# Kernel tuning notes

Hardware: AMD Instinct MI355X
Metric: run time of the kernel (lower is better)

## Reference

```python
import jax, jax.numpy as jnp
import numpy as np

B, N, K, C = 4, 8192, 16, 128
T = 3  # num_iterations


def _gather(x, idx):
    # x: (B, N, C), idx: (B, N, K) -> (B, N, K, C)
    return jax.vmap(lambda a, i: a[i])(x, idx)


def _linear(x, W, b):
    # torch nn.Linear convention: W is (out, in)
    return x @ W.T + b


def setup_inputs() -> dict:
    key = jax.random.key(0)
    ks = jax.random.split(key, 20)
    s = 0.05
    inp = {
        'xyz': jax.random.normal(ks[0], (B, N, 3), jnp.float32),
        'features': jax.random.normal(ks[1], (B, N, C), jnp.float32),
        'knn_idx': jax.random.randint(ks[2], (B, N, K), 0, N),
        # offset_pred: Linear(C,C) -> ReLU -> Linear(C,3)
        'off_W1': jax.random.normal(ks[3], (C, C), jnp.float32) * s,
        'off_b1': jnp.zeros((C,), jnp.float32),
        'off_W2': jax.random.normal(ks[4], (3, C), jnp.float32) * s,
        'off_b2': jnp.zeros((3,), jnp.float32),
        # per-iteration edge MLP: Linear(3+C, C) -> ReLU -> Linear(C, C)
        'edge_W1': jax.random.normal(ks[5], (T, C, 3 + C), jnp.float32) * s,
        'edge_b1': jnp.zeros((T, C), jnp.float32),
        'edge_W2': jax.random.normal(ks[6], (T, C, C), jnp.float32) * s,
        'edge_b2': jnp.zeros((T, C), jnp.float32),
        # per-iteration update MLP: Linear(2C, C) -> ReLU -> Linear(C, C)
        'upd_W1': jax.random.normal(ks[7], (T, C, 2 * C), jnp.float32) * s,
        'upd_b1': jnp.zeros((T, C), jnp.float32),
        'upd_W2': jax.random.normal(ks[8], (T, C, C), jnp.float32) * s,
        'upd_b2': jnp.zeros((T, C), jnp.float32),
    }
    return inp


def reference(xyz, features, knn_idx, off_W1, off_b1, off_W2, off_b2,
              edge_W1, edge_b1, edge_W2, edge_b2,
              upd_W1, upd_b1, upd_W2, upd_b2):
    n_iter = edge_W1.shape[0]
    for t in range(n_iter):
        delta_xyz = _linear(jax.nn.relu(_linear(features, off_W1, off_b1)), off_W2, off_b2)
        neighbor_xyz = _gather(xyz, knn_idx)          # (B,N,K,3)
        neighbor_feat = _gather(features, knn_idx)    # (B,N,K,C)
        center_xyz = xyz + delta_xyz                  # (B,N,3)
        rel_pos = neighbor_xyz - center_xyz[:, :, None, :]
        edge_input = jnp.concatenate([rel_pos, neighbor_feat], axis=-1)  # (B,N,K,3+C)
        edge_feat = _linear(jax.nn.relu(_linear(edge_input, edge_W1[t], edge_b1[t])), edge_W2[t], edge_b2[t])
        agg_feat = jnp.max(edge_feat, axis=2)         # (B,N,C)
        upd_in = jnp.concatenate([agg_feat, features], axis=-1)
        features = features + _linear(jax.nn.relu(_linear(upd_in, upd_W1[t], upd_b1[t])), upd_W2[t], upd_b2[t])
    return features
```

## Files before the change

### kernel.cpp

```cpp
#include <hip/hip_runtime.h>
#include <cstddef>

#define NB 4
#define NP 8192
#define NK 16
#define NC 128
#define HW_ 136
#define GIW 136
#define AGW 136
#define CW  132
#define UINW 264
#define HUW 136

using short8   = __attribute__((ext_vector_type(8))) short;
using ushort4v = __attribute__((ext_vector_type(4))) unsigned short;
using floatx4  = __attribute__((ext_vector_type(4))) float;

union U8 { short8 s8; unsigned u[4]; };

__device__ __forceinline__ unsigned short f2bf(float f) {
    union { float f; unsigned u; } v; v.f = f;
    unsigned r = v.u + 0x7FFFu + ((v.u >> 16) & 1u);
    return (unsigned short)(r >> 16);
}
__device__ __forceinline__ float bf2f(unsigned short u) {
    union { unsigned u; float f; } v; v.u = ((unsigned)u) << 16;
    return v.f;
}
__device__ __forceinline__ unsigned cvt_pk_bf16(float lo, float hi) {
    unsigned d;
    asm("v_cvt_pk_bf16_f32 %0, %1, %2" : "=v"(d) : "v"(lo), "v"(hi));
    return d;
}

#define MFMA(a, b, c) __builtin_amdgcn_mfma_f32_16x16x32_bf16((a), (b), (c), 0, 0, 0)

__device__ __forceinline__ short8 xform(short8 g, floatx4 ca, floatx4 cb) {
    U8 u;
    u.u[0] = cvt_pk_bf16(fmaxf(bf2f((unsigned short)g[0]) - ca[0], 0.f),
                         fmaxf(bf2f((unsigned short)g[1]) - ca[1], 0.f));
    u.u[1] = cvt_pk_bf16(fmaxf(bf2f((unsigned short)g[2]) - ca[2], 0.f),
                         fmaxf(bf2f((unsigned short)g[3]) - ca[3], 0.f));
    u.u[2] = cvt_pk_bf16(fmaxf(bf2f((unsigned short)g[4]) - cb[0], 0.f),
                         fmaxf(bf2f((unsigned short)g[5]) - cb[1], 0.f));
    u.u[3] = cvt_pk_bf16(fmaxf(bf2f((unsigned short)g[6]) - cb[2], 0.f),
                         fmaxf(bf2f((unsigned short)g[7]) - cb[3], 0.f));
    return u.s8;
}

__global__ void pack_weights_k(const float* __restrict__ offW1,
                               const float* __restrict__ eW1,
                               const float* __restrict__ eW2,
                               const float* __restrict__ uW1,
                               const float* __restrict__ uW2,
                               const float* __restrict__ eb1,
                               unsigned short* __restrict__ offW1p,
                               unsigned short* __restrict__ eW1fp,
                               unsigned short* __restrict__ eW2p,
                               unsigned short* __restrict__ uW1p,
                               unsigned short* __restrict__ uW2p,
                               float* __restrict__ eW1rTp)
{
    int i = blockIdx.x * 256 + threadIdx.x;
    if (i < 16384) { offW1p[i] = f2bf(offW1[i]); return; }
    i -= 16384;
    if (i < 49152) {
        int tt = i / 16384, rem = i % 16384;
        int o = rem / 128, k = rem % 128;
        eW1fp[i] = f2bf(eW1[(tt * 128 + o) * 131 + 3 + k]);
        return;
    }
    i -= 49152;
    if (i < 49152) { eW2p[i] = f2bf(eW2[i]); return; }
    i -= 49152;
    if (i < 98304) { uW1p[i] = f2bf(uW1[i]); return; }
    i -= 98304;
    if (i < 49152) { uW2p[i] = f2bf(uW2[i]); return; }
    i -= 49152;
    if (i < 1536) {
        int tt = i / 512, rem = i % 512;
        int j = rem / 128, col = rem % 128;
        eW1rTp[i] = (j < 3) ? eW1[(size_t)(tt * 128 + col) * 131 + j]
                            : eb1[tt * 128 + col];
    }
}

__global__ __launch_bounds__(256, 4)
void center_k(const float* __restrict__ Fin, const float* __restrict__ xyz,
              const unsigned short* __restrict__ offW1p,
              const float* __restrict__ offW2, const float* __restrict__ offb1,
              const float* __restrict__ offb2,
              const unsigned short* __restrict__ eW1fp,
              const float* __restrict__ eW1rT0,
              unsigned short* __restrict__ Gbf, float* __restrict__ ctr)
{
    __shared__ __align__(16) unsigned short sA[32 * HW_];
    __shared__ __align__(16) unsigned short sH[32 * HW_];
    __shared__ float s_XY[96];
    const int t = threadIdx.x, wv = t >> 6, ln = t & 63, q = ln >> 4, r = ln & 15;
    const int cg0 = wv << 1;
    const int base = blockIdx.x * 32;

    {
        int row = t >> 3, c16 = (t & 7) * 16;
        const float* src = Fin + (size_t)(base + row) * NC + c16;
        float4 f0 = *(const float4*)src;
        float4 f1 = *(const float4*)(src + 4);
        float4 f2 = *(const float4*)(src + 8);
        float4 f3 = *(const float4*)(src + 12);
        short8 u0, u1;
        u0[0]=f2bf(f0.x); u0[1]=f2bf(f0.y); u0[2]=f2bf(f0.z); u0[3]=f2bf(f0.w);
        u0[4]=f2bf(f1.x); u0[5]=f2bf(f1.y); u0[6]=f2bf(f1.z); u0[7]=f2bf(f1.w);
        u1[0]=f2bf(f2.x); u1[1]=f2bf(f2.y); u1[2]=f2bf(f2.z); u1[3]=f2bf(f2.w);
        u1[4]=f2bf(f3.x); u1[5]=f2bf(f3.y); u1[6]=f2bf(f3.z); u1[7]=f2bf(f3.w);
        *(short8*)&sA[row * HW_ + c16]     = u0;
        *(short8*)&sA[row * HW_ + c16 + 8] = u1;
    }
    if (t < 96) s_XY[t] = xyz[(size_t)base * 3 + t];
    __syncthreads();

    floatx4 agk[2][2];
    {
        short8 wo[2][4], wg[2][4];
#pragma unroll
        for (int c = 0; c < 2; ++c)
#pragma unroll
            for (int ks = 0; ks < 4; ++ks) {
                wo[c][ks] = *(const short8*)(offW1p + ((cg0 + c) * 16 + r) * NC + ks * 32 + q * 8);
                wg[c][ks] = *(const short8*)(eW1fp  + ((cg0 + c) * 16 + r) * NC + ks * 32 + q * 8);
            }
        float bo[2] = { offb1[cg0 * 16 + r], offb1[(cg0 + 1) * 16 + r] };
#pragma unroll
        for (int rt = 0; rt < 2; ++rt) {
            short8 af[4];
#pragma unroll
            for (int ks = 0; ks < 4; ++ks)
                af[ks] = *(const short8*)&sA[(rt * 16 + r) * HW_ + ks * 32 + q * 8];
            floatx4 ao[2] = { {0.f,0.f,0.f,0.f}, {0.f,0.f,0.f,0.f} };
            floatx4 ag[2] = { {0.f,0.f,0.f,0.f}, {0.f,0.f,0.f,0.f} };
#pragma unroll
            for (int c = 0; c < 2; ++c)
#pragma unroll
                for (int ks = 0; ks < 4; ++ks) {
                    ao[c] = MFMA(af[ks], wo[c][ks], ao[c]);
                    ag[c] = MFMA(af[ks], wg[c][ks], ag[c]);
                }
#pragma unroll
            for (int c = 0; c < 2; ++c) {
                int col = (cg0 + c) * 16 + r;
#pragma unroll
                for (int i = 0; i < 4; ++i)
                    sH[(rt * 16 + q * 4 + i) * HW_ + col] = f2bf(fmaxf(ao[c][i] + bo[c], 0.f));
                agk[rt][c] = ag[c];
            }
        }
    }
    __syncthreads();

    {
#pragma unroll
        for (int c = 0; c < 2; ++c) {
            int col = (cg0 + c) * 16 + r;
            float w0 = eW1rT0[col], w1 = eW1rT0[128 + col];
            float w2 = eW1rT0[256 + col], b1v = eW1rT0[384 + col];
#pragma unroll
            for (int rt = 0; rt < 2; ++rt)
#pragma unroll
                for (int i = 0; i < 4; ++i) {
                    int row = rt * 16 + q * 4 + i;
                    sA[row * HW_ + col] = f2bf(agk[rt][c][i]
                        + s_XY[row * 3 + 0] * w0 + s_XY[row * 3 + 1] * w1
                        + s_XY[row * 3 + 2] * w2 + b1v);
                }
        }
    }
    if (wv < 2) {
        int rt = wv;
        short8 wf[4];
#pragma unroll
        for (int ks = 0; ks < 4; ++ks) {
            short8 u = {0,0,0,0,0,0,0,0};
            if (r < 3) {
                const float* w = offW2 + r * NC + ks * 32 + q * 8;
                float4 f0 = *(const float4*)w;
                float4 f1 = *(const float4*)(w + 4);
                u[0]=f2bf(f0.x); u[1]=f2bf(f0.y); u[2]=f2bf(f0.z); u[3]=f2bf(f0.w);
                u[4]=f2bf(f1.x); u[5]=f2bf(f1.y); u[6]=f2bf(f1.z); u[7]=f2bf(f1.w);
            }
            wf[ks] = u;
        }
        short8 af[4];
#pragma unroll
        for (int ks = 0; ks < 4; ++ks)
            af[ks] = *(const short8*)&sH[(rt * 16 + r) * HW_ + ks * 32 + q * 8];
        floatx4 acc = {0.f, 0.f, 0.f, 0.f};
#pragma unroll
        for (int ks = 0; ks < 4; ++ks)
            acc = MFMA(af[ks], wf[ks], acc);
        if (r < 3) {
#pragma unroll
            for (int i = 0; i < 4; ++i) {
                int p = rt * 16 + q * 4 + i;
                ctr[(size_t)(base + p) * 3 + r] =
                    xyz[(size_t)(base + p) * 3 + r] + acc[i] + offb2[r];
            }
        }
    }
    __syncthreads();

    {
        int row = t >> 3, c16 = (t & 7) * 16;
        *(short8*)(Gbf + (size_t)(base + row) * NC + c16)     = *(short8*)&sA[row * HW_ + c16];
        *(short8*)(Gbf + (size_t)(base + row) * NC + c16 + 8) = *(short8*)&sA[row * HW_ + c16 + 8];
    }
}

__global__ __launch_bounds__(256, 2)
void edge_k(const unsigned short* __restrict__ Gbf,
            const int* __restrict__ knn,
            const float* __restrict__ ctr,
            const float* __restrict__ eW1rT,
            const float* __restrict__ eb2,
            const unsigned short* __restrict__ eW2p,
            unsigned short* __restrict__ aggG)
{
    __shared__ __align__(16) unsigned short s_H[64 * GIW];
    __shared__ __align__(16) float s_C[8 * CW];
    __shared__ __align__(16) unsigned short s_AGB[8 * AGW];

    const int xcd  = blockIdx.x & 7;
    const int slot = blockIdx.x >> 3;
    const int b    = xcd >> 1;
    const int n0   = ((slot << 1) | (xcd & 1)) << 3;
    const int t = threadIdx.x, wv = t >> 6, ln = t & 63;
    const int q = ln >> 4, r = ln & 15, cg0 = wv << 1;
    const int base = b * NP + n0;
    const int rr = t >> 4, c8 = (t & 15) * 8;

    const int* kb = knn + (size_t)base * NK;
    int kn[8];
#pragma unroll
    for (int j = 0; j < 8; ++j) kn[j] = kb[j * 16 + rr];
    short8 g0[4], g1[4];
#pragma unroll
    for (int p = 0; p < 4; ++p)
        g0[p] = *(const short8*)(Gbf + (size_t)(b * NP + kn[p]) * NC + c8);
#pragma unroll
    for (int p = 0; p < 4; ++p)
        g1[p] = *(const short8*)(Gbf + (size_t)(b * NP + kn[4 + p]) * NC + c8);

    short8 wf2[2][4];
#pragma unroll
    for (int c = 0; c < 2; ++c)
#pragma unroll
        for (int ks = 0; ks < 4; ++ks)
            wf2[c][ks] = *(const short8*)(eW2p + ((cg0 + c) * 16 + r) * NC + ks * 32 + q * 8);
    float eb2v[2] = { eb2[cg0 * 16 + r], eb2[(cg0 + 1) * 16 + r] };

    {
        int p = t >> 5, c0 = (t & 31) * 4;
        float cx = ctr[(size_t)(base + p) * 3 + 0];
        float cy = ctr[(size_t)(base + p) * 3 + 1];
        float cz = ctr[(size_t)(base + p) * 3 + 2];
        floatx4 w0 = *(const floatx4*)(eW1rT + c0);
        floatx4 w1 = *(const floatx4*)(eW1rT + 128 + c0);
        floatx4 w2 = *(const floatx4*)(eW1rT + 256 + c0);
#pragma unroll
        for (int k = 0; k < 4; ++k)
            s_C[p * CW + c0 + k] = cx * w0[k] + cy * w1[k] + cz * w2[k];
    }
    __syncthreads();

#pragma unroll
    for (int p = 0; p < 4; ++p) {
        const float* cp = &s_C[p * CW + c8];
        floatx4 ca = *(const floatx4*)(cp);
        floatx4 cb = *(const floatx4*)(cp + 4);
        *(short8*)&s_H[(p * 16 + rr) * GIW + c8] = xform(g0[p], ca, cb);
    }
    __syncthreads();

#pragma unroll
    for (int rt = 0; rt < 4; ++rt) {
        short8 af[4];
#pragma unroll
        for (int ks = 0; ks < 4; ++ks)
            af[ks] = *(const short8*)&s_H[(rt * 16 + r) * GIW + ks * 32 + q * 8];
        floatx4 acc[2] = { {0.f,0.f,0.f,0.f}, {0.f,0.f,0.f,0.f} };
#pragma unroll
        for (int c = 0; c < 2; ++c)
#pragma unroll
            for (int ks = 0; ks < 4; ++ks)
                acc[c] = MFMA(af[ks], wf2[c][ks], acc[c]);
#pragma unroll
        for (int c = 0; c < 2; ++c) {
            float m = fmaxf(fmaxf(acc[c][0], acc[c][1]), fmaxf(acc[c][2], acc[c][3]));
            m = fmaxf(m, __shfl_xor(m, 16));
            m = fmaxf(m, __shfl_xor(m, 32));
            if (q == 0)
                s_AGB[rt * AGW + (cg0 + c) * 16 + r] = f2bf(m + eb2v[c]);
        }
    }
    __syncthreads();

#pragma unroll
    for (int p = 0; p < 4; ++p) {
        const float* cp = &s_C[(4 + p) * CW + c8];
        floatx4 ca = *(const floatx4*)(cp);
        floatx4 cb = *(const floatx4*)(cp + 4);
        *(short8*)&s_H[(p * 16 + rr) * GIW + c8] = xform(g1[p], ca, cb);
    }
    __syncthreads();

#pragma unroll
    for (int rt = 0; rt < 4; ++rt) {
        short8 af[4];
#pragma unroll
        for (int ks = 0; ks < 4; ++ks)
            af[ks] = *(const short8*)&s_H[(rt * 16 + r) * GIW + ks * 32 + q * 8];
        floatx4 acc[2] = { {0.f,0.f,0.f,0.f}, {0.f,0.f,0.f,0.f} };
#pragma unroll
        for (int c = 0; c < 2; ++c)
#pragma unroll
            for (int ks = 0; ks < 4; ++ks)
                acc[c] = MFMA(af[ks], wf2[c][ks], acc[c]);
#pragma unroll
        for (int c = 0; c < 2; ++c) {
            float m = fmaxf(fmaxf(acc[c][0], acc[c][1]), fmaxf(acc[c][2], acc[c][3]));
            m = fmaxf(m, __shfl_xor(m, 16));
            m = fmaxf(m, __shfl_xor(m, 32));
            if (q == 0)
                s_AGB[(4 + rt) * AGW + (cg0 + c) * 16 + r] = f2bf(m + eb2v[c]);
        }
    }
    __syncthreads();

    if (t < 128) {
        int row = t >> 4, cc = (t & 15) * 8;
        *(short8*)(aggG + (size_t)(base + row) * NC + cc) = *(short8*)&s_AGB[row * AGW + cc];
    }
}

__global__ __launch_bounds__(256, 3)
void upd_k(const float* __restrict__ Fin, float* __restrict__ Fout,
           const unsigned short* __restrict__ aggG,
           const float* __restrict__ xyz,
           const unsigned short* __restrict__ uW1p,
           const unsigned short* __restrict__ uW2p,
           const float* __restrict__ ub1, const float* __restrict__ ub2,
           const unsigned short* __restrict__ eW1fpN,
           const float* __restrict__ eW1rTN,
           const unsigned short* __restrict__ offW1p,
           const float* __restrict__ offW2, const float* __restrict__ offb1,
           const float* __restrict__ offb2,
           unsigned short* __restrict__ Gbf, float* __restrict__ ctrOut,
           int doNext)
{
    __shared__ __align__(16) unsigned short s_UIN[32 * UINW];
    __shared__ __align__(16) unsigned short s_H[32 * HUW];
    __shared__ __align__(16) unsigned short s_FN[32 * HUW];
    __shared__ float s_XY[96];

    const int xcd  = blockIdx.x & 7;
    const int slot = blockIdx.x >> 3;
    const int b    = xcd >> 1;
    const int n0   = ((slot << 1) | (xcd & 1)) << 5;
    const int t = threadIdx.x, wv = t >> 6, ln = t & 63;
    const int q = ln >> 4, r = ln & 15, cg0 = wv << 1;
    const int base = b * NP + n0;
    const int row32 = t >> 3, c16 = (t & 7) * 16;

    {
        const unsigned short* ap = aggG + (size_t)(base + row32) * NC + c16;
        *(short8*)&s_UIN[row32 * UINW + c16]     = *(const short8*)ap;
        *(short8*)&s_UIN[row32 * UINW + c16 + 8] = *(const short8*)(ap + 8);
        const float* src = Fin + (size_t)(base + row32) * NC + c16;
        float4 f0 = *(const float4*)src;
        float4 f1 = *(const float4*)(src + 4);
        float4 f2 = *(const float4*)(src + 8);
        float4 f3 = *(const float4*)(src + 12);
        short8 u0, u1;
        u0[0]=f2bf(f0.x); u0[1]=f2bf(f0.y); u0[2]=f2bf(f0.z); u0[3]=f2bf(f0.w);
        u0[4]=f2bf(f1.x); u0[5]=f2bf(f1.y); u0[6]=f2bf(f1.z); u0[7]=f2bf(f1.w);
        u1[0]=f2bf(f2.x); u1[1]=f2bf(f2.y); u1[2]=f2bf(f2.z); u1[3]=f2bf(f2.w);
        u1[4]=f2bf(f3.x); u1[5]=f2bf(f3.y); u1[6]=f2bf(f3.z); u1[7]=f2bf(f3.w);
        *(short8*)&s_UIN[row32 * UINW + 128 + c16]     = u0;
        *(short8*)&s_UIN[row32 * UINW + 128 + c16 + 8] = u1;
    }
    if (t < 96) s_XY[t] = xyz[(size_t)base * 3 + t];
    __syncthreads();

    {
        short8 wfa[2][8];
#pragma unroll
        for (int c = 0; c < 2; ++c)
#pragma unroll
            for (int ks = 0; ks < 8; ++ks)
                wfa[c][ks] = *(const short8*)(uW1p + ((cg0 + c) * 16 + r) * 256 + ks * 32 + q * 8);
        float ub1v[2] = { ub1[cg0 * 16 + r], ub1[(cg0 + 1) * 16 + r] };
#pragma unroll
        for (int rt = 0; rt < 2; ++rt) {
            short8 af[8];
#pragma unroll
            for (int ks = 0; ks < 8; ++ks)
                af[ks] = *(const short8*)&s_UIN[(rt * 16 + r) * UINW + ks * 32 + q * 8];
            floatx4 acc3[2] = { {0.f,0.f,0.f,0.f}, {0.f,0.f,0.f,0.f} };
#pragma unroll
            for (int c = 0; c < 2; ++c)
#pragma unroll
                for (int ks = 0; ks < 8; ++ks)
                    acc3[c] = MFMA(af[ks], wfa[c][ks], acc3[c]);
#pragma unroll
            for (int c = 0; c < 2; ++c)
#pragma unroll
                for (int i = 0; i < 4; ++i)
                    s_H[(rt * 16 + q * 4 + i) * HUW + (cg0 + c) * 16 + r] =
                        f2bf(fmaxf(acc3[c][i] + ub1v[c], 0.f));
        }
    }
    __syncthreads();

    {
        short8 wfb[2][4];
#pragma unroll
        for (int c = 0; c < 2; ++c)
#pragma unroll
            for (int ks = 0; ks < 4; ++ks)
                wfb[c][ks] = *(const short8*)(uW2p + ((cg0 + c) * 16 + r) * NC + ks * 32 + q * 8);
        float ub2v[2] = { ub2[cg0 * 16 + r], ub2[(cg0 + 1) * 16 + r] };
#pragma unroll
        for (int rt = 0; rt < 2; ++rt) {
            short8 af[4];
#pragma unroll
            for (int ks = 0; ks < 4; ++ks)
                af[ks] = *(const short8*)&s_H[(rt * 16 + r) * HUW + ks * 32 + q * 8];
            floatx4 acc[2] = { {0.f,0.f,0.f,0.f}, {0.f,0.f,0.f,0.f} };
#pragma unroll
            for (int c = 0; c < 2; ++c)
#pragma unroll
                for (int ks = 0; ks < 4; ++ks)
                    acc[c] = MFMA(af[ks], wfb[c][ks], acc[c]);
#pragma unroll
            for (int c = 0; c < 2; ++c) {
                int col = (cg0 + c) * 16 + r;
#pragma unroll
                for (int i = 0; i < 4; ++i) {
                    int p = rt * 16 + q * 4 + i;
                    float fnew = Fin[(size_t)(base + p) * NC + col] + acc[c][i] + ub2v[c];
                    Fout[(size_t)(base + p) * NC + col] = fnew;
                    s_FN[p * HUW + col] = f2bf(fnew);
                }
            }
        }
    }

    if (doNext) {
        __syncthreads();
        {
            short8 wg[2][4], wo[2][4];
#pragma unroll
            for (int c = 0; c < 2; ++c)
#pragma unroll
                for (int ks = 0; ks < 4; ++ks) {
                    wg[c][ks] = *(const short8*)(eW1fpN + ((cg0 + c) * 16 + r) * NC + ks * 32 + q * 8);
                    wo[c][ks] = *(const short8*)(offW1p + ((cg0 + c) * 16 + r) * NC + ks * 32 + q * 8);
                }
            float bo[2] = { offb1[cg0 * 16 + r], offb1[(cg0 + 1) * 16 + r] };
#pragma unroll
            for (int rt = 0; rt < 2; ++rt) {
                short8 af[4];
#pragma unroll
                for (int ks = 0; ks < 4; ++ks)
                    af[ks] = *(const short8*)&s_FN[(rt * 16 + r) * HUW + ks * 32 + q * 8];
                floatx4 ag[2] = { {0.f,0.f,0.f,0.f}, {0.f,0.f,0.f,0.f} };
                floatx4 ao[2] = { {0.f,0.f,0.f,0.f}, {0.f,0.f,0.f,0.f} };
#pragma unroll
                for (int c = 0; c < 2; ++c)
#pragma unroll
                    for (int ks = 0; ks < 4; ++ks) {
                        ag[c] = MFMA(af[ks], wg[c][ks], ag[c]);
                        ao[c] = MFMA(af[ks], wo[c][ks], ao[c]);
                    }
#pragma unroll
                for (int c = 0; c < 2; ++c) {
                    int col = (cg0 + c) * 16 + r;
                    float w0 = eW1rTN[col], w1 = eW1rTN[128 + col];
                    float w2 = eW1rTN[256 + col], b1v = eW1rTN[384 + col];
#pragma unroll
                    for (int i = 0; i < 4; ++i) {
                        int p = rt * 16 + q * 4 + i;
                        s_UIN[p * UINW + col] = f2bf(ag[c][i]
                            + s_XY[p * 3 + 0] * w0 + s_XY[p * 3 + 1] * w1
                            + s_XY[p * 3 + 2] * w2 + b1v);
                        s_H[p * HUW + col]    = f2bf(fmaxf(ao[c][i] + bo[c], 0.f));
                    }
                }
            }
        }
        __syncthreads();

        *(short8*)(Gbf + (size_t)(base + row32) * NC + c16) =
            *(short8*)&s_UIN[row32 * UINW + c16];
        *(short8*)(Gbf + (size_t)(base + row32) * NC + c16 + 8) =
            *(short8*)&s_UIN[row32 * UINW + c16 + 8];

        if (wv < 2) {
            int rt = wv;
            short8 wf[4];
#pragma unroll
            for (int ks = 0; ks < 4; ++ks) {
                short8 u = {0,0,0,0,0,0,0,0};
                if (r < 3) {
                    const float* w = offW2 + r * NC + ks * 32 + q * 8;
                    float4 f0 = *(const float4*)w;
                    float4 f1 = *(const float4*)(w + 4);
                    u[0]=f2bf(f0.x); u[1]=f2bf(f0.y); u[2]=f2bf(f0.z); u[3]=f2bf(f0.w);
                    u[4]=f2bf(f1.x); u[5]=f2bf(f1.y); u[6]=f2bf(f1.z); u[7]=f2bf(f1.w);
                }
                wf[ks] = u;
            }
            short8 af[4];
#pragma unroll
            for (int ks = 0; ks < 4; ++ks)
                af[ks] = *(const short8*)&s_H[(rt * 16 + r) * HUW + ks * 32 + q * 8];
            floatx4 acc = {0.f, 0.f, 0.f, 0.f};
#pragma unroll
            for (int ks = 0; ks < 4; ++ks)
                acc = MFMA(af[ks], wf[ks], acc);
            if (r < 3) {
#pragma unroll
                for (int i = 0; i < 4; ++i) {
                    int p = rt * 16 + q * 4 + i;
                    ctrOut[(size_t)(base + p) * 3 + r] =
                        xyz[(size_t)(base + p) * 3 + r] + acc[i] + offb2[r];
                }
            }
        }
    }
}

extern "C" void kernel_launch(void* const* d_in, const int* in_sizes, int n_in,
                              void* d_out, int out_size, void* d_ws, size_t ws_size,
                              hipStream_t stream)
{
    const float* xyz   = (const float*)d_in[0];
    const float* feat  = (const float*)d_in[1];
    const int*   knn   = (const int*)d_in[2];
    const float* offW1 = (const float*)d_in[3];
    const float* offb1 = (const float*)d_in[4];
    const float* offW2 = (const float*)d_in[5];
    const float* offb2 = (const float*)d_in[6];
    const float* eW1   = (const float*)d_in[7];
    const float* eb1   = (const float*)d_in[8];
    const float* eW2   = (const float*)d_in[9];
    const float* eb2   = (const float*)d_in[10];
    const float* uW1   = (const float*)d_in[11];
    const float* ub1   = (const float*)d_in[12];
    const float* uW2   = (const float*)d_in[13];
    const float* ub2   = (const float*)d_in[14];
    float* out = (float*)d_out;

    char* ws = (char*)d_ws;
    unsigned short* Gbf    = (unsigned short*)ws;
    float*          ctrb   = (float*)(ws + 8388608);
    unsigned short* offW1p = (unsigned short*)(ws + 8781824);
    unsigned short* eW1fp  = (unsigned short*)(ws + 8814592);
    unsigned short* eW2p   = (unsigned short*)(ws + 8912896);
    unsigned short* uW1p   = (unsigned short*)(ws + 9011200);
    unsigned short* uW2p   = (unsigned short*)(ws + 9207808);
    unsigned short* aggG   = (unsigned short*)(ws + 9306112);
    float*          eW1rTp = (float*)(ws + 17694720);

    pack_weights_k<<<1030, 256, 0, stream>>>(offW1, eW1, eW2, uW1, uW2, eb1,
                                             offW1p, eW1fp, eW2p, uW1p, uW2p,
                                             eW1rTp);

    center_k<<<1024, 256, 0, stream>>>(feat, xyz, offW1p, offW2,
                                       offb1, offb2, eW1fp, eW1rTp,
                                       Gbf, ctrb);

    for (int tt = 0; tt < 3; ++tt) {
        int ntt = (tt + 1) % 3;
        edge_k<<<4096, 256, 0, stream>>>(
            Gbf, knn, ctrb,
            eW1rTp + tt * 512, eb2 + tt * 128,
            eW2p + tt * 16384, aggG);
        const float* fin = (tt == 0) ? feat : out;
        upd_k<<<1024, 256, 0, stream>>>(
            fin, out, aggG, xyz,
            uW1p + tt * 32768, uW2p + tt * 16384, ub1 + tt * 128, ub2 + tt * 128,
            eW1fp + ntt * 16384, eW1rTp + ntt * 512,
            offW1p, offW2, offb1, offb2,
            Gbf, ctrb, (tt < 2) ? 1 : 0);
    }
}
```

Before: 278.9 us.

## Process two point groups per edge block and prefetch second group's neighbor gathers

Each edge_k block now handles 16 points (two 8-point groups) instead of 8, so the grid halves. The per-block cost of loading the edge_W2 MFMA fragments and biases is spread over twice as much work. The second group's neighbor feature gathers are issued before the first group's MFMA phases so their latency overlaps compute. In exchange the kernel holds more registers (extra knn indices and gathered vectors) and uses a larger shared center buffer, which may reduce occupancy.

```diff
diff --git a/kernel.cpp b/kernel.cpp
--- a/kernel.cpp
+++ b/kernel.cpp
@@ -225,29 +225,27 @@
             unsigned short* __restrict__ aggG)
 {
     __shared__ __align__(16) unsigned short s_H[64 * GIW];
-    __shared__ __align__(16) float s_C[8 * CW];
+    __shared__ __align__(16) float s_C[16 * CW];
     __shared__ __align__(16) unsigned short s_AGB[8 * AGW];
 
     const int xcd  = blockIdx.x & 7;
     const int slot = blockIdx.x >> 3;
     const int b    = xcd >> 1;
-    const int n0   = ((slot << 1) | (xcd & 1)) << 3;
+    const int base0 = b * NP + ((((slot << 1) | 0) << 1 | (xcd & 1)) << 3);
+    const int base1 = b * NP + ((((slot << 1) | 1) << 1 | (xcd & 1)) << 3);
     const int t = threadIdx.x, wv = t >> 6, ln = t & 63;
     const int q = ln >> 4, r = ln & 15, cg0 = wv << 1;
-    const int base = b * NP + n0;
     const int rr = t >> 4, c8 = (t & 15) * 8;
 
-    const int* kb = knn + (size_t)base * NK;
-    int kn[8];
-#pragma unroll
-    for (int j = 0; j < 8; ++j) kn[j] = kb[j * 16 + rr];
-    short8 g0[4], g1[4];
-#pragma unroll
-    for (int p = 0; p < 4; ++p)
-        g0[p] = *(const short8*)(Gbf + (size_t)(b * NP + kn[p]) * NC + c8);
-#pragma unroll
-    for (int p = 0; p < 4; ++p)
-        g1[p] = *(const short8*)(Gbf + (size_t)(b * NP + kn[4 + p]) * NC + c8);
+    const int* kb0 = knn + (size_t)base0 * NK;
+    const int* kb1 = knn + (size_t)base1 * NK;
+    int kn0[8], kn1[8];
+#pragma unroll
+    for (int j = 0; j < 8; ++j) { kn0[j] = kb0[j * 16 + rr]; kn1[j] = kb1[j * 16 + rr]; }
+    short8 gA[8];
+#pragma unroll
+    for (int p = 0; p < 8; ++p)
+        gA[p] = *(const short8*)(Gbf + (size_t)(b * NP + kn0[p]) * NC + c8);
 
     short8 wf2[2][4];
 #pragma unroll
@@ -258,28 +256,37 @@
     float eb2v[2] = { eb2[cg0 * 16 + r], eb2[(cg0 + 1) * 16 + r] };
 
     {
-        int p = t >> 5, c0 = (t & 31) * 4;
-        float cx = ctr[(size_t)(base + p) * 3 + 0];
-        float cy = ctr[(size_t)(base + p) * 3 + 1];
-        float cz = ctr[(size_t)(base + p) * 3 + 2];
-        floatx4 w0 = *(const floatx4*)(eW1rT + c0);
-        floatx4 w1 = *(const floatx4*)(eW1rT + 128 + c0);
-        floatx4 w2 = *(const floatx4*)(eW1rT + 256 + c0);
-#pragma unroll
-        for (int k = 0; k < 4; ++k)
-            s_C[p * CW + c0 + k] = cx * w0[k] + cy * w1[k] + cz * w2[k];
+        int p16 = t >> 4, c0 = (t & 15) * 8;
+        int pb = (p16 < 8) ? (base0 + p16) : (base1 + (p16 - 8));
+        float cx = ctr[(size_t)pb * 3 + 0];
+        float cy = ctr[(size_t)pb * 3 + 1];
+        float cz = ctr[(size_t)pb * 3 + 2];
+        floatx4 w0a = *(const floatx4*)(eW1rT + c0);
+        floatx4 w0b = *(const floatx4*)(eW1rT + c0 + 4);
+        floatx4 w1a = *(const floatx4*)(eW1rT + 128 + c0);
+        floatx4 w1b = *(const floatx4*)(eW1rT + 128 + c0 + 4);
+        floatx4 w2a = *(const floatx4*)(eW1rT + 256 + c0);
+        floatx4 w2b = *(const floatx4*)(eW1rT + 256 + c0 + 4);
+#pragma unroll
+        for (int k = 0; k < 4; ++k) {
+            s_C[p16 * CW + c0 + k]     = cx * w0a[k] + cy * w1a[k] + cz * w2a[k];
+            s_C[p16 * CW + c0 + 4 + k] = cx * w0b[k] + cy * w1b[k] + cz * w2b[k];
+        }
     }
     __syncthreads();
 
 #pragma unroll
     for (int p = 0; p < 4; ++p) {
         const float* cp = &s_C[p * CW + c8];
-        floatx4 ca = *(const floatx4*)(cp);
-        floatx4 cb = *(const floatx4*)(cp + 4);
-        *(short8*)&s_H[(p * 16 + rr) * GIW + c8] = xform(g0[p], ca, cb);
-    }
-    __syncthreads();
-
+        *(short8*)&s_H[(p * 16 + rr) * GIW + c8] =
+            xform(gA[p], *(const floatx4*)cp, *(const floatx4*)(cp + 4));
+    }
+    __syncthreads();
+
+    short8 gB0[4];
+#pragma unroll
+    for (int p = 0; p < 4; ++p)
+        gB0[p] = *(const short8*)(Gbf + (size_t)(b * NP + kn1[p]) * NC + c8);
 #pragma unroll
     for (int rt = 0; rt < 4; ++rt) {
         short8 af[4];
@@ -306,12 +313,15 @@
 #pragma unroll
     for (int p = 0; p < 4; ++p) {
         const float* cp = &s_C[(4 + p) * CW + c8];
-        floatx4 ca = *(const floatx4*)(cp);
-        floatx4 cb = *(const floatx4*)(cp + 4);
-        *(short8*)&s_H[(p * 16 + rr) * GIW + c8] = xform(g1[p], ca, cb);
-    }
-    __syncthreads();
-
+        *(short8*)&s_H[(p * 16 + rr) * GIW + c8] =
+            xform(gA[4 + p], *(const floatx4*)cp, *(const floatx4*)(cp + 4));
+    }
+    __syncthreads();
+
+    short8 gB1[4];
+#pragma unroll
+    for (int p = 0; p < 4; ++p)
+        gB1[p] = *(const short8*)(Gbf + (size_t)(b * NP + kn1[4 + p]) * NC + c8);
 #pragma unroll
     for (int rt = 0; rt < 4; ++rt) {
         short8 af[4];
@@ -337,7 +347,73 @@
 
     if (t < 128) {
         int row = t >> 4, cc = (t & 15) * 8;
-        *(short8*)(aggG + (size_t)(base + row) * NC + cc) = *(short8*)&s_AGB[row * AGW + cc];
+        *(short8*)(aggG + (size_t)(base0 + row) * NC + cc) = *(short8*)&s_AGB[row * AGW + cc];
+    }
+#pragma unroll
+    for (int p = 0; p < 4; ++p) {
+        const float* cp = &s_C[(8 + p) * CW + c8];
+        *(short8*)&s_H[(p * 16 + rr) * GIW + c8] =
+            xform(gB0[p], *(const floatx4*)cp, *(const floatx4*)(cp + 4));
+    }
+    __syncthreads();
+
+#pragma unroll
+    for (int rt = 0; rt < 4; ++rt) {
+        short8 af[4];
+#pragma unroll
+        for (int ks = 0; ks < 4; ++ks)
+            af[ks] = *(const short8*)&s_H[(rt * 16 + r) * GIW + ks * 32 + q * 8];
+        floatx4 acc[2] = { {0.f,0.f,0.f,0.f}, {0.f,0.f,0.f,0.f} };
+#pragma unroll
+        for (int c = 0; c < 2; ++c)
+#pragma unroll
+            for (int ks = 0; ks < 4; ++ks)
+                acc[c] = MFMA(af[ks], wf2[c][ks], acc[c]);
+#pragma unroll
+        for (int c = 0; c < 2; ++c) {
+            float m = fmaxf(fmaxf(acc[c][0], acc[c][1]), fmaxf(acc[c][2], acc[c][3]));
+            m = fmaxf(m, __shfl_xor(m, 16));
+            m = fmaxf(m, __shfl_xor(m, 32));
+            if (q == 0)
+                s_AGB[rt * AGW + (cg0 + c) * 16 + r] = f2bf(m + eb2v[c]);
+        }
+    }
+    __syncthreads();
+
+#pragma unroll
+    for (int p = 0; p < 4; ++p) {
+        const float* cp = &s_C[(12 + p) * CW + c8];
+        *(short8*)&s_H[(p * 16 + rr) * GIW + c8] =
+            xform(gB1[p], *(const floatx4*)cp, *(const floatx4*)(cp + 4));
+    }
+    __syncthreads();
+
+#pragma unroll
+    for (int rt = 0; rt < 4; ++rt) {
+        short8 af[4];
+#pragma unroll
+        for (int ks = 0; ks < 4; ++ks)
+            af[ks] = *(const short8*)&s_H[(rt * 16 + r) * GIW + ks * 32 + q * 8];
+        floatx4 acc[2] = { {0.f,0.f,0.f,0.f}, {0.f,0.f,0.f,0.f} };
+#pragma unroll
+        for (int c = 0; c < 2; ++c)
+#pragma unroll
+            for (int ks = 0; ks < 4; ++ks)
+                acc[c] = MFMA(af[ks], wf2[c][ks], acc[c]);
+#pragma unroll
+        for (int c = 0; c < 2; ++c) {
+            float m = fmaxf(fmaxf(acc[c][0], acc[c][1]), fmaxf(acc[c][2], acc[c][3]));
+            m = fmaxf(m, __shfl_xor(m, 16));
+            m = fmaxf(m, __shfl_xor(m, 32));
+            if (q == 0)
+                s_AGB[(4 + rt) * AGW + (cg0 + c) * 16 + r] = f2bf(m + eb2v[c]);
+        }
+    }
+    __syncthreads();
+
+    if (t < 128) {
+        int row = t >> 4, cc = (t & 15) * 8;
+        *(short8*)(aggG + (size_t)(base1 + row) * NC + cc) = *(short8*)&s_AGB[row * AGW + cc];
     }
 }
 
@@ -581,7 +657,7 @@
 
     for (int tt = 0; tt < 3; ++tt) {
         int ntt = (tt + 1) % 3;
-        edge_k<<<4096, 256, 0, stream>>>(
+        edge_k<<<2048, 256, 0, stream>>>(
             Gbf, knn, ctrb,
             eW1rTp + tt * 512, eb2 + tt * 128,
             eW2p + tt * 16384, aggG);
```

After: 279.5 us. No clear change (+0.2%).
